# Kernel optimization log

Hardware: AMD Instinct MI355X
Metric: run time of the kernel (lower is better)

Reference implementation:

```python
import jax, jax.numpy as jnp
import numpy as np
import math

N_HEAD = 8
D_MODEL = 512
HEAD_SIZE = D_MODEL // N_HEAD
VOCAB = 16384
BLOCK = 512
LN_EPS = 1e-5


def sinusoidal_pe(max_len, dim):
    pos = np.arange(max_len)[:, None].astype(np.float32)
    div = np.exp(np.arange(0, dim, 2).astype(np.float32) * (-math.log(10000.0) / dim))
    pe = np.zeros((max_len, dim), dtype=np.float32)
    pe[:, 0::2] = np.sin(pos * div)
    pe[:, 1::2] = np.cos(pos * div)
    return jnp.asarray(pe)  # (max_len, hs)


def setup_inputs() -> dict:
    key = jax.random.key(0)
    ks = jax.random.split(key, 6)
    b, t = 4, BLOCK
    return {
        "x": jax.random.normal(ks[0], (b, t, 1), dtype=jnp.float32),
        "embedding": jax.random.normal(ks[1], (N_HEAD, VOCAB, HEAD_SIZE), dtype=jnp.float32),
        "enc_w": jax.random.normal(ks[2], (D_MODEL, 1), dtype=jnp.float32) * 0.05,
        "enc_b": jax.random.normal(ks[3], (D_MODEL,), dtype=jnp.float32) * 0.05,
        "ln_w": jnp.ones((HEAD_SIZE,), dtype=jnp.float32),
        "ln_b": jnp.zeros((HEAD_SIZE,), dtype=jnp.float32),
        "dec_w": jax.random.normal(ks[4], (1, D_MODEL), dtype=jnp.float32) * 0.05,
        "dec_b": jax.random.normal(ks[5], (1,), dtype=jnp.float32) * 0.05,
    }


def reference(x, embedding, enc_w, enc_b, ln_w, ln_b, dec_w, dec_b):
    b, t, _ = x.shape
    # encoder: Linear(input_dim -> d_model)
    h = x @ enc_w.T + enc_b                              # (b, t, d_model)
    h = h.reshape(b, t, N_HEAD, HEAD_SIZE).transpose(0, 2, 1, 3)  # (b, nh, t, hs)
    # sinusoidal positional encoding over time, added to head dim
    h = h + sinusoidal_pe(BLOCK, HEAD_SIZE)[:t]
    # LayerNorm over hs
    mu = h.mean(-1, keepdims=True)
    var = ((h - mu) ** 2).mean(-1, keepdims=True)
    h = (h - mu) * jax.lax.rsqrt(var + LN_EPS) * ln_w + ln_b
    # attention over shared per-head codebook
    scores = jnp.einsum('bnth,nvh->bntv', h, embedding) / math.sqrt(D_MODEL)
    probs = jax.nn.softmax(scores, axis=-1)              # (b, nh, t, vocab)
    quant = jnp.einsum('bntv,nvh->bnth', probs, embedding)
    quant = quant.transpose(0, 2, 1, 3).reshape(b, t, D_MODEL)
    # decoder: Linear(d_model -> output_dim)
    return quant @ dec_w.T + dec_b                       # (b, t, 1)
```

## Files before the change

### kernel.cpp

```cpp
#include <hip/hip_runtime.h>
#include <hip/hip_bf16.h>
#include <math.h>

#define NH 8
#define HS 64
#define VOCAB 16384
#define QPH 2048
#define NSLICE 32
#define QSCALE (0.04419417382415922f * 1.4426950408889634f)

typedef __attribute__((ext_vector_type(8))) short bf16x8;
typedef __attribute__((ext_vector_type(4))) float f32x4;

static __device__ __forceinline__ unsigned short f2bf(float f) {
    __hip_bfloat16 h = __float2bfloat16(f);
    unsigned short u;
    __builtin_memcpy(&u, &h, 2);
    return u;
}

static __device__ __forceinline__ float fexp2(float x) {
#if __has_builtin(__builtin_amdgcn_exp2f)
    return __builtin_amdgcn_exp2f(x);
#else
    return __expf(x * 0.6931471805599453f);
#endif
}

__global__ void eprep(const float* __restrict__ emb, const float* __restrict__ dec_w,
                      unsigned short* __restrict__ ebf, float* __restrict__ g) {
    int i4  = blockIdx.x * 256 + threadIdx.x;
    int row = i4 >> 4;
    int c   = i4 & 15;
    int n   = row >> 14;
    f32x4 v = ((const f32x4*)emb)[i4];
    ushort4 u = make_ushort4(f2bf(v.x), f2bf(v.y), f2bf(v.z), f2bf(v.w));
    ((ushort4*)ebf)[i4] = u;
    const float* dw = dec_w + n * 64 + c * 4;
    float p = v.x * dw[0] + v.y * dw[1] + v.z * dw[2] + v.w * dw[3];
    p += __shfl_xor(p, 1); p += __shfl_xor(p, 2);
    p += __shfl_xor(p, 4); p += __shfl_xor(p, 8);
    if (c == 0) g[row] = p;
}

__global__ void qprep(const float* __restrict__ x, const float* __restrict__ enc_w,
                      const float* __restrict__ enc_b, const float* __restrict__ ln_w,
                      const float* __restrict__ ln_b, unsigned short* __restrict__ qbf) {
    int row  = blockIdx.x * 4 + (threadIdx.x >> 6);
    int h    = threadIdx.x & 63;
    int n = row >> 11;
    int q = row & 2047;
    int t = q & 511;
    float xv = x[q];
    int d = n * 64 + h;
    float h2  = (float)(h & ~1);
    float div = __expf(h2 * (-9.210340371976184f / 64.0f));
    float ang = (float)t * div;
    float pe  = (h & 1) ? __cosf(ang) : __sinf(ang);
    float v = xv * enc_w[d] + enc_b[d] + pe;
    float s = v;
    #pragma unroll
    for (int off = 1; off < 64; off <<= 1) s += __shfl_xor(s, off);
    float mu = s * (1.0f / 64.0f);
    float dd = v - mu;
    float s2 = dd * dd;
    #pragma unroll
    for (int off = 1; off < 64; off <<= 1) s2 += __shfl_xor(s2, off);
    float var = s2 * (1.0f / 64.0f);
    float y = dd * rsqrtf(var + 1e-5f) * ln_w[h] + ln_b[h];
    qbf[row * 64 + h] = f2bf(y * QSCALE);
}

__global__ void __launch_bounds__(256, 3)
attn(const unsigned short* __restrict__ qbf, const unsigned short* __restrict__ ebf,
     const float* __restrict__ g, float2* __restrict__ part) {
    int tid  = threadIdx.x;
    int w    = tid >> 6;
    int lane = tid & 63;
    int quad = lane >> 4;
    int l15  = lane & 15;
    int head   = blockIdx.x & 7;
    int vslice = (blockIdx.x >> 3) & 31;
    int qchunk = blockIdx.x >> 8;
    int qbase  = (qchunk * 4 + w) * 128;

    const short* qp = (const short*)qbf + (size_t)(head * QPH + qbase) * HS;
    bf16x8 qf[8][2];
    #pragma unroll
    for (int qt = 0; qt < 8; ++qt) {
        const short* qrow = qp + (qt * 16 + l15) * HS + quad * 8;
        qf[qt][0] = *(const bf16x8*)(qrow);
        qf[qt][1] = *(const bf16x8*)(qrow + 32);
    }

    const short* ep = (const short*)ebf + ((size_t)head * VOCAB + vslice * 512) * HS;
    const float* gp = g + head * VOCAB + vslice * 512;

    float num[8] = {0.f, 0.f, 0.f, 0.f, 0.f, 0.f, 0.f, 0.f};
    float den[8] = {0.f, 0.f, 0.f, 0.f, 0.f, 0.f, 0.f, 0.f};
    const f32x4 z = {0.f, 0.f, 0.f, 0.f};

    #pragma clang loop unroll(disable)
    for (int it = 0; it < 16; ++it) {
        int vb = it * 32;
        const short* e0 = ep + (size_t)(vb + l15) * HS + quad * 8;
        const short* e1 = ep + (size_t)(vb + 16 + l15) * HS + quad * 8;
        bf16x8 a00 = *(const bf16x8*)(e0);
        bf16x8 a01 = *(const bf16x8*)(e0 + 32);
        bf16x8 a10 = *(const bf16x8*)(e1);
        bf16x8 a11 = *(const bf16x8*)(e1 + 32);
        f32x4 gv0 = *(const f32x4*)(gp + vb + quad * 4);
        f32x4 gv1 = *(const f32x4*)(gp + vb + 16 + quad * 4);
        #pragma unroll
        for (int qt = 0; qt < 8; ++qt) {
            f32x4 acc0 = __builtin_amdgcn_mfma_f32_16x16x32_bf16(a00, qf[qt][0], z, 0, 0, 0);
            acc0       = __builtin_amdgcn_mfma_f32_16x16x32_bf16(a01, qf[qt][1], acc0, 0, 0, 0);
            f32x4 acc1 = __builtin_amdgcn_mfma_f32_16x16x32_bf16(a10, qf[qt][0], z, 0, 0, 0);
            acc1       = __builtin_amdgcn_mfma_f32_16x16x32_bf16(a11, qf[qt][1], acc1, 0, 0, 0);
            #pragma unroll
            for (int r = 0; r < 4; ++r) {
                float p0 = fexp2(acc0[r]);
                float p1 = fexp2(acc1[r]);
                den[qt] += p0 + p1;
                num[qt] += p0 * gv0[r] + p1 * gv1[r];
            }
        }
    }

    #pragma unroll
    for (int qt = 0; qt < 8; ++qt) {
        num[qt] += __shfl_xor(num[qt], 16); num[qt] += __shfl_xor(num[qt], 32);
        den[qt] += __shfl_xor(den[qt], 16); den[qt] += __shfl_xor(den[qt], 32);
    }
    #pragma unroll
    for (int j = 0; j < 2; ++j) {
        int qt = quad * 2 + j;
        int qg = qbase + qt * 16 + l15;
        part[((size_t)vslice * NH + head) * QPH + qg] = make_float2(num[qt], den[qt]);
    }
}

__global__ void fin(const float2* __restrict__ part, const float* __restrict__ dec_b,
                    float* __restrict__ out) {
    __shared__ float red[8][32];
    int t  = threadIdx.x;
    int ql = t & 31;
    int n  = t >> 5;
    int q  = blockIdx.x * 32 + ql;
    float nv = 0.f, dv = 0.f;
    #pragma unroll 8
    for (int sl = 0; sl < NSLICE; ++sl) {
        float2 nd = part[((size_t)sl * NH + n) * QPH + q];
        nv += nd.x; dv += nd.y;
    }
    red[n][ql] = nv / dv;
    __syncthreads();
    if (t < 32) {
        float s = dec_b[0];
        #pragma unroll
        for (int m = 0; m < NH; ++m) s += red[m][t];
        out[q] = s;
    }
}

extern "C" void kernel_launch(void* const* d_in, const int* in_sizes, int n_in,
                              void* d_out, int out_size, void* d_ws, size_t ws_size,
                              hipStream_t stream) {
    const float* x     = (const float*)d_in[0];
    const float* emb   = (const float*)d_in[1];
    const float* enc_w = (const float*)d_in[2];
    const float* enc_b = (const float*)d_in[3];
    const float* ln_w  = (const float*)d_in[4];
    const float* ln_b  = (const float*)d_in[5];
    const float* dec_w = (const float*)d_in[6];
    const float* dec_b = (const float*)d_in[7];
    float* out = (float*)d_out;

    char* ws = (char*)d_ws;
    unsigned short* qbf  = (unsigned short*)(ws);
    unsigned short* ebf  = (unsigned short*)(ws + 2097152);
    float*          g    = (float*)(ws + 2097152 + 16777216);
    float2*         part = (float2*)(ws + 2097152 + 16777216 + 524288);

    hipLaunchKernelGGL(eprep, dim3(8192), dim3(256), 0, stream, emb, dec_w, ebf, g);
    hipLaunchKernelGGL(qprep, dim3(4096), dim3(256), 0, stream, x, enc_w, enc_b, ln_w, ln_b, qbf);
    hipLaunchKernelGGL(attn,  dim3(1024), dim3(256), 0, stream, qbf, ebf, g, part);
    hipLaunchKernelGGL(fin,   dim3(64),   dim3(256), 0, stream, part, dec_b, out);
}
```

Baseline: 150.8 us.

## Fuse embedding bf16 conversion and decoder projection into attention kernel

Drops the separate eprep pass, which converted the fp32 codebook to bf16 and computed per-row decoder projections into workspace. The attention kernel now loads fp32 embedding rows directly, converts them to bf16 in registers, and computes the dec_w dot product with cross-lane shuffles. This removes one launch and the write and re-read of the 16 MB bf16 copy. In exchange each codebook slice is read as fp32 by four query-chunk blocks, so global traffic doubles unless cached. The conversion and projection ALU work is also repeated per block, and register pressure goes up.

```diff
diff --git a/kernel.cpp b/kernel.cpp
--- a/kernel.cpp
+++ b/kernel.cpp
@@ -12,11 +12,14 @@
 typedef __attribute__((ext_vector_type(8))) short bf16x8;
 typedef __attribute__((ext_vector_type(4))) float f32x4;
 
-static __device__ __forceinline__ unsigned short f2bf(float f) {
+static __device__ __forceinline__ unsigned short f2bfu(float f) {
     __hip_bfloat16 h = __float2bfloat16(f);
     unsigned short u;
     __builtin_memcpy(&u, &h, 2);
     return u;
+}
+static __device__ __forceinline__ short f2bfs(float f) {
+    return (short)f2bfu(f);
 }
 
 static __device__ __forceinline__ float fexp2(float x) {
@@ -25,22 +28,6 @@
 #else
     return __expf(x * 0.6931471805599453f);
 #endif
-}
-
-__global__ void eprep(const float* __restrict__ emb, const float* __restrict__ dec_w,
-                      unsigned short* __restrict__ ebf, float* __restrict__ g) {
-    int i4  = blockIdx.x * 256 + threadIdx.x;
-    int row = i4 >> 4;
-    int c   = i4 & 15;
-    int n   = row >> 14;
-    f32x4 v = ((const f32x4*)emb)[i4];
-    ushort4 u = make_ushort4(f2bf(v.x), f2bf(v.y), f2bf(v.z), f2bf(v.w));
-    ((ushort4*)ebf)[i4] = u;
-    const float* dw = dec_w + n * 64 + c * 4;
-    float p = v.x * dw[0] + v.y * dw[1] + v.z * dw[2] + v.w * dw[3];
-    p += __shfl_xor(p, 1); p += __shfl_xor(p, 2);
-    p += __shfl_xor(p, 4); p += __shfl_xor(p, 8);
-    if (c == 0) g[row] = p;
 }
 
 __global__ void qprep(const float* __restrict__ x, const float* __restrict__ enc_w,
@@ -68,12 +55,12 @@
     for (int off = 1; off < 64; off <<= 1) s2 += __shfl_xor(s2, off);
     float var = s2 * (1.0f / 64.0f);
     float y = dd * rsqrtf(var + 1e-5f) * ln_w[h] + ln_b[h];
-    qbf[row * 64 + h] = f2bf(y * QSCALE);
+    qbf[row * 64 + h] = f2bfu(y * QSCALE);
 }
 
 __global__ void __launch_bounds__(256, 3)
-attn(const unsigned short* __restrict__ qbf, const unsigned short* __restrict__ ebf,
-     const float* __restrict__ g, float2* __restrict__ part) {
+attn(const unsigned short* __restrict__ qbf, const float* __restrict__ emb,
+     const float* __restrict__ dec_w, float2* __restrict__ part) {
     int tid  = threadIdx.x;
     int w    = tid >> 6;
     int lane = tid & 63;
@@ -93,8 +80,15 @@
         qf[qt][1] = *(const bf16x8*)(qrow + 32);
     }
 
-    const short* ep = (const short*)ebf + ((size_t)head * VOCAB + vslice * 512) * HS;
-    const float* gp = g + head * VOCAB + vslice * 512;
+    const float* dwh = dec_w + head * 64;
+    float dwf[16];
+    #pragma unroll
+    for (int j = 0; j < 8; ++j) {
+        dwf[j]     = dwh[quad * 8 + j];
+        dwf[8 + j] = dwh[32 + quad * 8 + j];
+    }
+
+    const float* ep32 = emb + ((size_t)head * VOCAB + vslice * 512) * HS;
 
     float num[8] = {0.f, 0.f, 0.f, 0.f, 0.f, 0.f, 0.f, 0.f};
     float den[8] = {0.f, 0.f, 0.f, 0.f, 0.f, 0.f, 0.f, 0.f};
@@ -103,14 +97,43 @@
     #pragma clang loop unroll(disable)
     for (int it = 0; it < 16; ++it) {
         int vb = it * 32;
-        const short* e0 = ep + (size_t)(vb + l15) * HS + quad * 8;
-        const short* e1 = ep + (size_t)(vb + 16 + l15) * HS + quad * 8;
-        bf16x8 a00 = *(const bf16x8*)(e0);
-        bf16x8 a01 = *(const bf16x8*)(e0 + 32);
-        bf16x8 a10 = *(const bf16x8*)(e1);
-        bf16x8 a11 = *(const bf16x8*)(e1 + 32);
-        f32x4 gv0 = *(const f32x4*)(gp + vb + quad * 4);
-        f32x4 gv1 = *(const f32x4*)(gp + vb + 16 + quad * 4);
+        const float* p0r = ep32 + (size_t)(vb + l15) * HS;
+        const float* p1r = ep32 + (size_t)(vb + 16 + l15) * HS;
+        f32x4 r0a = *(const f32x4*)(p0r + quad * 8);
+        f32x4 r0b = *(const f32x4*)(p0r + quad * 8 + 4);
+        f32x4 r0c = *(const f32x4*)(p0r + 32 + quad * 8);
+        f32x4 r0d = *(const f32x4*)(p0r + 32 + quad * 8 + 4);
+        f32x4 r1a = *(const f32x4*)(p1r + quad * 8);
+        f32x4 r1b = *(const f32x4*)(p1r + quad * 8 + 4);
+        f32x4 r1c = *(const f32x4*)(p1r + 32 + quad * 8);
+        f32x4 r1d = *(const f32x4*)(p1r + 32 + quad * 8 + 4);
+
+        bf16x8 a00, a01, a10, a11;
+        #pragma unroll
+        for (int j = 0; j < 4; ++j) {
+            a00[j] = f2bfs(r0a[j]); a00[4 + j] = f2bfs(r0b[j]);
+            a01[j] = f2bfs(r0c[j]); a01[4 + j] = f2bfs(r0d[j]);
+            a10[j] = f2bfs(r1a[j]); a10[4 + j] = f2bfs(r1b[j]);
+            a11[j] = f2bfs(r1c[j]); a11[4 + j] = f2bfs(r1d[j]);
+        }
+
+        float pr0 = 0.f, pr1 = 0.f;
+        #pragma unroll
+        for (int j = 0; j < 4; ++j) {
+            pr0 += r0a[j] * dwf[j] + r0b[j] * dwf[4 + j]
+                 + r0c[j] * dwf[8 + j] + r0d[j] * dwf[12 + j];
+            pr1 += r1a[j] * dwf[j] + r1b[j] * dwf[4 + j]
+                 + r1c[j] * dwf[8 + j] + r1d[j] * dwf[12 + j];
+        }
+        pr0 += __shfl_xor(pr0, 16); pr0 += __shfl_xor(pr0, 32);
+        pr1 += __shfl_xor(pr1, 16); pr1 += __shfl_xor(pr1, 32);
+        f32x4 gv0, gv1;
+        #pragma unroll
+        for (int r = 0; r < 4; ++r) {
+            gv0[r] = __shfl(pr0, quad * 20 + r);
+            gv1[r] = __shfl(pr1, quad * 20 + r);
+        }
+
         #pragma unroll
         for (int qt = 0; qt < 8; ++qt) {
             f32x4 acc0 = __builtin_amdgcn_mfma_f32_16x16x32_bf16(a00, qf[qt][0], z, 0, 0, 0);
@@ -178,12 +201,9 @@
 
     char* ws = (char*)d_ws;
     unsigned short* qbf  = (unsigned short*)(ws);
-    unsigned short* ebf  = (unsigned short*)(ws + 2097152);
-    float*          g    = (float*)(ws + 2097152 + 16777216);
-    float2*         part = (float2*)(ws + 2097152 + 16777216 + 524288);
-
-    hipLaunchKernelGGL(eprep, dim3(8192), dim3(256), 0, stream, emb, dec_w, ebf, g);
+    float2*         part = (float2*)(ws + 2097152);
+
     hipLaunchKernelGGL(qprep, dim3(4096), dim3(256), 0, stream, x, enc_w, enc_b, ln_w, ln_b, qbf);
-    hipLaunchKernelGGL(attn,  dim3(1024), dim3(256), 0, stream, qbf, ebf, g, part);
+    hipLaunchKernelGGL(attn,  dim3(1024), dim3(256), 0, stream, qbf, emb, dec_w, part);
     hipLaunchKernelGGL(fin,   dim3(64),   dim3(256), 0, stream, part, dec_b, out);
 }
```

Measured after the change: 161.9 us. +7.4%, slower.

## Stage codebook slice in padded LDS and split vocab into more slices

Applied to the files above, without the earlier changes.

The attention kernel now copies a 256-row slice of the bf16 codebook and its decoder projections into padded shared memory once per block. All four waves then read their MFMA operands from LDS instead of each loading the same rows from global memory. The vocabulary is split into 64 slices instead of 32, the grid doubles, and the occupancy hint rises to 4 blocks per CU, which should even out the wave tail. The cost is a sync and staging prologue per block and twice as many partial sums for the final reduction to read.

```diff
diff --git a/kernel.cpp b/kernel.cpp
--- a/kernel.cpp
+++ b/kernel.cpp
@@ -6,13 +6,15 @@
 #define HS 64
 #define VOCAB 16384
 #define QPH 2048
-#define NSLICE 32
+#define NSLICE 64
+#define SROWS 256
+#define LPAD 72
 #define QSCALE (0.04419417382415922f * 1.4426950408889634f)
 
 typedef __attribute__((ext_vector_type(8))) short bf16x8;
 typedef __attribute__((ext_vector_type(4))) float f32x4;
 
-static __device__ __forceinline__ unsigned short f2bf(float f) {
+static __device__ __forceinline__ unsigned short f2bfu(float f) {
     __hip_bfloat16 h = __float2bfloat16(f);
     unsigned short u;
     __builtin_memcpy(&u, &h, 2);
@@ -34,7 +36,7 @@
     int c   = i4 & 15;
     int n   = row >> 14;
     f32x4 v = ((const f32x4*)emb)[i4];
-    ushort4 u = make_ushort4(f2bf(v.x), f2bf(v.y), f2bf(v.z), f2bf(v.w));
+    ushort4 u = make_ushort4(f2bfu(v.x), f2bfu(v.y), f2bfu(v.z), f2bfu(v.w));
     ((ushort4*)ebf)[i4] = u;
     const float* dw = dec_w + n * 64 + c * 4;
     float p = v.x * dw[0] + v.y * dw[1] + v.z * dw[2] + v.w * dw[3];
@@ -68,21 +70,36 @@
     for (int off = 1; off < 64; off <<= 1) s2 += __shfl_xor(s2, off);
     float var = s2 * (1.0f / 64.0f);
     float y = dd * rsqrtf(var + 1e-5f) * ln_w[h] + ln_b[h];
-    qbf[row * 64 + h] = f2bf(y * QSCALE);
-}
-
-__global__ void __launch_bounds__(256, 3)
+    qbf[row * 64 + h] = f2bfu(y * QSCALE);
+}
+
+__global__ void __launch_bounds__(256, 4)
 attn(const unsigned short* __restrict__ qbf, const unsigned short* __restrict__ ebf,
      const float* __restrict__ g, float2* __restrict__ part) {
+    __shared__ short Es[SROWS * LPAD];
+    __shared__ float Gs[SROWS];
+
     int tid  = threadIdx.x;
     int w    = tid >> 6;
     int lane = tid & 63;
     int quad = lane >> 4;
     int l15  = lane & 15;
     int head   = blockIdx.x & 7;
-    int vslice = (blockIdx.x >> 3) & 31;
-    int qchunk = blockIdx.x >> 8;
+    int vslice = (blockIdx.x >> 3) & 63;
+    int qchunk = blockIdx.x >> 9;
     int qbase  = (qchunk * 4 + w) * 128;
+
+    const short* eg = (const short*)ebf + ((size_t)head * VOCAB + vslice * SROWS) * HS;
+    const float* gp = g + head * VOCAB + vslice * SROWS;
+    #pragma unroll
+    for (int j = 0; j < 8; ++j) {
+        int idx = j * 256 + tid;
+        int row = idx >> 3;
+        int c8  = idx & 7;
+        bf16x8 v = *(const bf16x8*)(eg + row * HS + c8 * 8);
+        *(bf16x8*)(&Es[row * LPAD + c8 * 8]) = v;
+    }
+    Gs[tid] = gp[tid];
 
     const short* qp = (const short*)qbf + (size_t)(head * QPH + qbase) * HS;
     bf16x8 qf[8][2];
@@ -93,24 +110,23 @@
         qf[qt][1] = *(const bf16x8*)(qrow + 32);
     }
 
-    const short* ep = (const short*)ebf + ((size_t)head * VOCAB + vslice * 512) * HS;
-    const float* gp = g + head * VOCAB + vslice * 512;
+    __syncthreads();
 
     float num[8] = {0.f, 0.f, 0.f, 0.f, 0.f, 0.f, 0.f, 0.f};
     float den[8] = {0.f, 0.f, 0.f, 0.f, 0.f, 0.f, 0.f, 0.f};
     const f32x4 z = {0.f, 0.f, 0.f, 0.f};
 
     #pragma clang loop unroll(disable)
-    for (int it = 0; it < 16; ++it) {
+    for (int it = 0; it < 8; ++it) {
         int vb = it * 32;
-        const short* e0 = ep + (size_t)(vb + l15) * HS + quad * 8;
-        const short* e1 = ep + (size_t)(vb + 16 + l15) * HS + quad * 8;
+        const short* e0 = &Es[(vb + l15) * LPAD + quad * 8];
+        const short* e1 = &Es[(vb + 16 + l15) * LPAD + quad * 8];
         bf16x8 a00 = *(const bf16x8*)(e0);
         bf16x8 a01 = *(const bf16x8*)(e0 + 32);
         bf16x8 a10 = *(const bf16x8*)(e1);
         bf16x8 a11 = *(const bf16x8*)(e1 + 32);
-        f32x4 gv0 = *(const f32x4*)(gp + vb + quad * 4);
-        f32x4 gv1 = *(const f32x4*)(gp + vb + 16 + quad * 4);
+        f32x4 gv0 = *(const f32x4*)(&Gs[vb + quad * 4]);
+        f32x4 gv1 = *(const f32x4*)(&Gs[vb + 16 + quad * 4]);
         #pragma unroll
         for (int qt = 0; qt < 8; ++qt) {
             f32x4 acc0 = __builtin_amdgcn_mfma_f32_16x16x32_bf16(a00, qf[qt][0], z, 0, 0, 0);
@@ -184,6 +200,6 @@
 
     hipLaunchKernelGGL(eprep, dim3(8192), dim3(256), 0, stream, emb, dec_w, ebf, g);
     hipLaunchKernelGGL(qprep, dim3(4096), dim3(256), 0, stream, x, enc_w, enc_b, ln_w, ln_b, qbf);
-    hipLaunchKernelGGL(attn,  dim3(1024), dim3(256), 0, stream, qbf, ebf, g, part);
+    hipLaunchKernelGGL(attn,  dim3(2048), dim3(256), 0, stream, qbf, ebf, g, part);
     hipLaunchKernelGGL(fin,   dim3(64),   dim3(256), 0, stream, part, dec_b, out);
 }
```

Result: slower. 155.3 us (+3.0%).
